# Performance work log

Measured on AMD Instinct MI355X. Metric: run time of the kernel, lower is better.

## Reference

```python
import jax, jax.numpy as jnp
import numpy as np

TAG_DIM = 1
EPS = 1e-6
LOSS_WEIGHTS = (0.001, 0.001, 1.0)


def setup_inputs() -> dict:
    key = jax.random.key(0)
    k1, k2, k3, k4 = jax.random.split(key, 4)
    B, S, n_parts, H, W = 8, 4, 17, 128, 128
    C = (1 + TAG_DIM) * n_parts
    L = n_parts * H * W
    preds = jax.random.normal(k1, (B, S, C, H, W), dtype=jnp.float32)
    masks = jax.random.uniform(k2, (B, H, W), dtype=jnp.float32)
    heatmaps = jax.random.uniform(k3, (B, n_parts, H, W), dtype=jnp.float32)
    keypoints = jax.random.randint(k4, (B, 30, n_parts, 2), 0, L, dtype=jnp.int64)
    return {"preds": preds, "masks": masks, "heatmaps": heatmaps, "keypoints": keypoints}


def reference(preds, masks, heatmaps, keypoints):
    B, S, C, H, W = preds.shape
    n_parts = heatmaps.shape[1]
    dets = preds[:, :, :n_parts]                                   # [B,S,P_joints,H,W]
    tags = preds[:, :, n_parts:(1 + TAG_DIM) * n_parts].reshape(B, S, TAG_DIM, -1)  # [B,S,T,L]

    idx = keypoints[..., 0]              # [B,P,J] flat indices into L
    vis = keypoints[..., 1] > 0          # [B,P,J]

    # ragged gather of tag embeddings per keypoint, vmapped over images
    g = jax.vmap(lambda t, i: jnp.take(t, i, axis=-1))(tags, idx)  # [B,S,T,P,J]

    vmask = vis[:, None, None].astype(tags.dtype)                  # [B,1,1,P,J]
    cnt = vis.sum(-1).astype(tags.dtype)                           # [B,P] valid joints per person
    person_valid = cnt > 0                                         # [B,P]
    safe_cnt = jnp.maximum(cnt, 1.0)

    # per-person mean tag (pull center)
    mean = (g * vmask).sum(-1) / safe_cnt[:, None, None]           # [B,S,T,P]
    # pull: mean over (valid joints x tag_dim) of squared deviation, summed over persons
    pull_pp = (((g - mean[..., None]) ** 2) * vmask).sum(axis=(2, 4)) / (safe_cnt[:, None] * TAG_DIM)  # [B,S,P]
    num = person_valid.sum(-1).astype(tags.dtype)                  # [B]
    pull = (pull_pp * person_valid[:, None].astype(tags.dtype)).sum(-1) / (num[:, None] + EPS)  # [B,S]

    # push: pairwise exp(-||mean_p - mean_q||^2) over valid person pairs
    D = ((mean[..., :, None] - mean[..., None, :]) ** 2).sum(axis=2)  # [B,S,P,P]
    pm = (person_valid[:, None, :, None] & person_valid[:, None, None, :]).astype(tags.dtype)  # [B,1,P,P]
    push_sum = (jnp.exp(-D) * pm).sum(axis=(2, 3)) - num[:, None]
    push = push_sum / (((num - 1.0) * num + EPS)[:, None]) * 0.5    # [B,S]

    # heatmap detection loss
    det = (((dets - heatmaps[:, None]) ** 2) * masks[:, None, None]).mean(axis=(2, 3, 4))  # [B,S]

    loss = (LOSS_WEIGHTS[0] * push.mean()
            + LOSS_WEIGHTS[1] * pull.mean()
            + LOSS_WEIGHTS[2] * det.mean())
    return loss
```

## Files before the change

### kernel.cpp

```cpp
#include <hip/hip_runtime.h>

#define HW     16384
#define NP     17
#define CCH    34
#define BB     8
#define SS     4
#define NPERS  30
#define NBS    (BB*SS)
#define NDET4  (NBS*NP*(HW/4))
#define DETBLOCKS 1088
#define LOSS_EPS 1e-6f

__device__ __forceinline__ float block_reduce_sum(float v, float* sred) {
    for (int off = 32; off > 0; off >>= 1)
        v += __shfl_down(v, off, 64);
    const int lane = threadIdx.x & 63;
    const int wave = threadIdx.x >> 6;
    if (lane == 0) sred[wave] = v;
    __syncthreads();
    if (threadIdx.x == 0) {
        float s = 0.f;
        const int nw = blockDim.x >> 6;
        for (int i = 0; i < nw; i++) s += sred[i];
        sred[0] = s;
    }
    __syncthreads();
    return sred[0];
}

__global__ __launch_bounds__(256) void k_det(const float* __restrict__ preds,
                                             const float* __restrict__ masks,
                                             const float* __restrict__ heat,
                                             float* __restrict__ partial) {
    __shared__ float sred[4];
    float acc = 0.f;
    const int stride = gridDim.x * blockDim.x;
    for (int e4 = blockIdx.x * blockDim.x + threadIdx.x; e4 < NDET4; e4 += stride) {
        const int hw4   = e4 & ((HW / 4) - 1);
        const int plane = e4 >> 12;
        const int bs    = plane / NP;
        const int p     = plane - bs * NP;
        const int b     = bs >> 2;
        const float4 d = *(const float4*)(preds + ((size_t)bs * CCH + p) * HW + (size_t)hw4 * 4);
        const float4 h = *(const float4*)(heat  + ((size_t)b * NP + p) * HW + (size_t)hw4 * 4);
        const float4 m = *(const float4*)(masks + (size_t)b * HW + (size_t)hw4 * 4);
        float dx = d.x - h.x, dy = d.y - h.y, dz = d.z - h.z, dw = d.w - h.w;
        acc += dx * dx * m.x + dy * dy * m.y + dz * dz * m.z + dw * dw * m.w;
    }
    float tot = block_reduce_sum(acc, sred);
    if (threadIdx.x == 0) partial[blockIdx.x] = tot;
}

__global__ __launch_bounds__(256) void k_group(const float* __restrict__ preds,
                                               const int* __restrict__ kp,
                                               float* __restrict__ pull_out,
                                               float* __restrict__ push_out) {
    __shared__ float sg[NPERS * NP];
    __shared__ float svis[NPERS * NP];
    __shared__ float smean[NPERS];
    __shared__ float scnt[NPERS];
    __shared__ float spull[NPERS];
    __shared__ float sred[4];
    __shared__ float snum;

    const int bs = blockIdx.x;
    const int b  = bs >> 2;
    const int tid = threadIdx.x;
    const size_t tag_base = ((size_t)bs * CCH + NP) * HW;

    for (int t = tid; t < NPERS * NP; t += 256) {
        const int kbase = (b * NPERS * NP + t) * 2;
        int ii = kp[kbase];
        const int vv = kp[kbase + 1];
        if (ii < 0) ii = 0;
        if (ii >= NP * HW) ii = NP * HW - 1;
        svis[t] = (vv > 0) ? 1.f : 0.f;
        sg[t]   = preds[tag_base + (size_t)ii];
    }
    __syncthreads();

    if (tid < NPERS) {
        float c = 0.f, msum = 0.f;
        for (int k = 0; k < NP; k++) {
            c    += svis[tid * NP + k];
            msum += sg[tid * NP + k] * svis[tid * NP + k];
        }
        const float sc = fmaxf(c, 1.f);
        const float m = msum / sc;
        float pp = 0.f;
        for (int k = 0; k < NP; k++) {
            const float dd = sg[tid * NP + k] - m;
            pp += dd * dd * svis[tid * NP + k];
        }
        scnt[tid]  = c;
        smean[tid] = m;
        spull[tid] = pp / sc;
    }
    __syncthreads();

    if (tid == 0) {
        float num = 0.f, psum = 0.f;
        for (int i = 0; i < NPERS; i++) {
            if (scnt[i] > 0.f) { num += 1.f; psum += spull[i]; }
        }
        snum = num;
        pull_out[bs] = psum / (num + LOSS_EPS);
    }
    __syncthreads();

    float pacc = 0.f;
    for (int t = tid; t < NPERS * NPERS; t += 256) {
        const int i = t / NPERS;
        const int j = t - i * NPERS;
        const float vi = (scnt[i] > 0.f) ? 1.f : 0.f;
        const float vj = (scnt[j] > 0.f) ? 1.f : 0.f;
        const float d = smean[i] - smean[j];
        pacc += expf(-d * d) * vi * vj;
    }
    const float ptot = block_reduce_sum(pacc, sred);
    if (tid == 0) {
        const float num = snum;
        push_out[bs] = (ptot - num) / ((num - 1.f) * num + LOSS_EPS) * 0.5f;
    }
}

__global__ __launch_bounds__(256) void k_final(const float* __restrict__ partial,
                                               const float* __restrict__ pull_v,
                                               const float* __restrict__ push_v,
                                               float* __restrict__ out) {
    __shared__ float sred[4];
    float a = 0.f;
    for (int i = threadIdx.x; i < DETBLOCKS; i += 256) a += partial[i];
    const float det_sum = block_reduce_sum(a, sred);
    if (threadIdx.x == 0) {
        float pl = 0.f, ph = 0.f;
        for (int i = 0; i < NBS; i++) { pl += pull_v[i]; ph += push_v[i]; }
        const float det_mean = det_sum / (float)((size_t)NBS * NP * HW);
        const float loss = 0.001f * (ph / (float)NBS)
                         + 0.001f * (pl / (float)NBS)
                         + det_mean;
        out[0] = loss;
    }
}

extern "C" void kernel_launch(void* const* d_in, const int* in_sizes, int n_in,
                              void* d_out, int out_size, void* d_ws, size_t ws_size,
                              hipStream_t stream) {
    const float* preds = (const float*)d_in[0];
    const float* masks = (const float*)d_in[1];
    const float* heat  = (const float*)d_in[2];
    const int*   kp    = (const int*)d_in[3];
    float* out = (float*)d_out;
    float* ws  = (float*)d_ws;
    k_det<<<DETBLOCKS, 256, 0, stream>>>(preds, masks, heat, ws);
    k_group<<<NBS, 256, 0, stream>>>(preds, kp, ws + DETBLOCKS, ws + DETBLOCKS + NBS);
    k_final<<<1, 256, 0, stream>>>(ws, ws + DETBLOCKS, ws + DETBLOCKS + NBS, out);
}
```

Measured before the change: 113.2 us.

## Fuse det, group and final kernels into one launch with last-block reduction

Merges the three kernels into a single grid: the first blocks compute the detection loss, 32 extra blocks compute the pull/push terms, and the last block to finish (found with an atomic counter) does the final reduction. The detection loop is also restructured so each thread loads heatmap and mask once and reuses them across the 4 stacks, cutting redundant reads of those tensors. This removes two kernel launches and their gaps, at the cost of a memset and an atomic-based completion protocol.

```diff
diff --git a/kernel.cpp b/kernel.cpp
--- a/kernel.cpp
+++ b/kernel.cpp
@@ -1,17 +1,24 @@
 #include <hip/hip_runtime.h>
 
-#define HW     16384
-#define NP     17
-#define CCH    34
-#define BB     8
-#define SS     4
-#define NPERS  30
-#define NBS    (BB*SS)
-#define NDET4  (NBS*NP*(HW/4))
-#define DETBLOCKS 1088
+#define HW      16384
+#define HW4     4096
+#define NP      17
+#define CCH     34
+#define BB      8
+#define SS      4
+#define NPERS   30
+#define NBS     (BB*SS)
+#define DETB    1088
+#define GROUPB  32
+#define GRID    (DETB + GROUPB)
+#define DITEMS  (NP*BB*HW4)
 #define LOSS_EPS 1e-6f
 
+#define WS_PART 16
+#define WS_PP   (WS_PART + DETB)
+
 __device__ __forceinline__ float block_reduce_sum(float v, float* sred) {
+    __syncthreads();
     for (int off = 32; off > 0; off >>= 1)
         v += __shfl_down(v, off, 64);
     const int lane = threadIdx.x & 63;
@@ -20,126 +27,138 @@
     __syncthreads();
     if (threadIdx.x == 0) {
         float s = 0.f;
-        const int nw = blockDim.x >> 6;
-        for (int i = 0; i < nw; i++) s += sred[i];
+        for (int i = 0; i < 4; i++) s += sred[i];
         sred[0] = s;
     }
     __syncthreads();
     return sred[0];
 }
 
-__global__ __launch_bounds__(256) void k_det(const float* __restrict__ preds,
-                                             const float* __restrict__ masks,
-                                             const float* __restrict__ heat,
-                                             float* __restrict__ partial) {
+__global__ __launch_bounds__(256) void k_fused(const float* __restrict__ preds,
+                                               const float* __restrict__ masks,
+                                               const float* __restrict__ heat,
+                                               const int*   __restrict__ kp,
+                                               float* __restrict__ out,
+                                               float* __restrict__ ws,
+                                               unsigned* __restrict__ counter) {
     __shared__ float sred[4];
-    float acc = 0.f;
-    const int stride = gridDim.x * blockDim.x;
-    for (int e4 = blockIdx.x * blockDim.x + threadIdx.x; e4 < NDET4; e4 += stride) {
-        const int hw4   = e4 & ((HW / 4) - 1);
-        const int plane = e4 >> 12;
-        const int bs    = plane / NP;
-        const int p     = plane - bs * NP;
-        const int b     = bs >> 2;
-        const float4 d = *(const float4*)(preds + ((size_t)bs * CCH + p) * HW + (size_t)hw4 * 4);
-        const float4 h = *(const float4*)(heat  + ((size_t)b * NP + p) * HW + (size_t)hw4 * 4);
-        const float4 m = *(const float4*)(masks + (size_t)b * HW + (size_t)hw4 * 4);
-        float dx = d.x - h.x, dy = d.y - h.y, dz = d.z - h.z, dw = d.w - h.w;
-        acc += dx * dx * m.x + dy * dy * m.y + dz * dz * m.z + dw * dw * m.w;
-    }
-    float tot = block_reduce_sum(acc, sred);
-    if (threadIdx.x == 0) partial[blockIdx.x] = tot;
-}
-
-__global__ __launch_bounds__(256) void k_group(const float* __restrict__ preds,
-                                               const int* __restrict__ kp,
-                                               float* __restrict__ pull_out,
-                                               float* __restrict__ push_out) {
     __shared__ float sg[NPERS * NP];
     __shared__ float svis[NPERS * NP];
     __shared__ float smean[NPERS];
     __shared__ float scnt[NPERS];
     __shared__ float spull[NPERS];
-    __shared__ float sred[4];
     __shared__ float snum;
+    __shared__ int   slast;
 
-    const int bs = blockIdx.x;
-    const int b  = bs >> 2;
     const int tid = threadIdx.x;
-    const size_t tag_base = ((size_t)bs * CCH + NP) * HW;
+    const int bid = blockIdx.x;
 
-    for (int t = tid; t < NPERS * NP; t += 256) {
-        const int kbase = (b * NPERS * NP + t) * 2;
-        int ii = kp[kbase];
-        const int vv = kp[kbase + 1];
-        if (ii < 0) ii = 0;
-        if (ii >= NP * HW) ii = NP * HW - 1;
-        svis[t] = (vv > 0) ? 1.f : 0.f;
-        sg[t]   = preds[tag_base + (size_t)ii];
+    if (bid < DETB) {
+        float acc = 0.f;
+        const int t0 = bid * 256 + tid;
+        #pragma unroll
+        for (int it = 0; it < 2; ++it) {
+            const int t    = t0 + it * (DETB * 256);
+            const int hw4  = t & (HW4 - 1);
+            const int rest = t >> 12;
+            const int b    = rest / NP;
+            const int p    = rest - b * NP;
+            const float4 h = *(const float4*)(heat  + ((size_t)rest) * HW + (size_t)hw4 * 4);
+            const float4 m = *(const float4*)(masks + (size_t)b * HW + (size_t)hw4 * 4);
+            #pragma unroll
+            for (int s = 0; s < SS; s++) {
+                const int bs = b * SS + s;
+                const float4 d = *(const float4*)(preds + ((size_t)bs * CCH + p) * HW + (size_t)hw4 * 4);
+                const float dx = d.x - h.x, dy = d.y - h.y, dz = d.z - h.z, dw = d.w - h.w;
+                acc += dx * dx * m.x + dy * dy * m.y + dz * dz * m.z + dw * dw * m.w;
+            }
+        }
+        const float tot = block_reduce_sum(acc, sred);
+        if (tid == 0) ws[WS_PART + bid] = tot;
+    } else {
+        const int bs = bid - DETB;
+        const int b  = bs >> 2;
+        const size_t tag_base = ((size_t)bs * CCH + NP) * HW;
+
+        for (int t = tid; t < NPERS * NP; t += 256) {
+            const int kbase = (b * NPERS * NP + t) * 2;
+            int ii = kp[kbase];
+            const int vv = kp[kbase + 1];
+            if (ii < 0) ii = 0;
+            if (ii >= NP * HW) ii = NP * HW - 1;
+            svis[t] = (vv > 0) ? 1.f : 0.f;
+            sg[t]   = preds[tag_base + (size_t)ii];
+        }
+        __syncthreads();
+
+        if (tid < NPERS) {
+            float c = 0.f, msum = 0.f;
+            for (int k = 0; k < NP; k++) {
+                c    += svis[tid * NP + k];
+                msum += sg[tid * NP + k] * svis[tid * NP + k];
+            }
+            const float sc = fmaxf(c, 1.f);
+            const float mu = msum / sc;
+            float pp = 0.f;
+            for (int k = 0; k < NP; k++) {
+                const float dd = sg[tid * NP + k] - mu;
+                pp += dd * dd * svis[tid * NP + k];
+            }
+            scnt[tid]  = c;
+            smean[tid] = mu;
+            spull[tid] = pp / sc;
+        }
+        __syncthreads();
+
+        if (tid == 0) {
+            float num = 0.f, psum = 0.f;
+            for (int i = 0; i < NPERS; i++)
+                if (scnt[i] > 0.f) { num += 1.f; psum += spull[i]; }
+            snum = num;
+            ws[WS_PP + bs] = psum / (num + LOSS_EPS);
+        }
+        __syncthreads();
+
+        float pacc = 0.f;
+        for (int t = tid; t < NPERS * NPERS; t += 256) {
+            const int i = t / NPERS;
+            const int j = t - i * NPERS;
+            const float vi = (scnt[i] > 0.f) ? 1.f : 0.f;
+            const float vj = (scnt[j] > 0.f) ? 1.f : 0.f;
+            const float d = smean[i] - smean[j];
+            pacc += expf(-d * d) * vi * vj;
+        }
+        const float ptot = block_reduce_sum(pacc, sred);
+        if (tid == 0) {
+            const float num = snum;
+            ws[WS_PP + NBS + bs] = (ptot - num) / ((num - 1.f) * num + LOSS_EPS) * 0.5f;
+        }
+    }
+
+    __syncthreads();
+    if (tid == 0) {
+        __threadfence();
+        const unsigned old = __hip_atomic_fetch_add(counter, 1u,
+                                __ATOMIC_ACQ_REL, __HIP_MEMORY_SCOPE_AGENT);
+        slast = (old == GRID - 1) ? 1 : 0;
     }
     __syncthreads();
 
-    if (tid < NPERS) {
-        float c = 0.f, msum = 0.f;
-        for (int k = 0; k < NP; k++) {
-            c    += svis[tid * NP + k];
-            msum += sg[tid * NP + k] * svis[tid * NP + k];
+    if (slast) {
+        float a = 0.f;
+        for (int i = tid; i < DETB; i += 256)
+            a += __hip_atomic_load(&ws[WS_PART + i], __ATOMIC_RELAXED,
+                                   __HIP_MEMORY_SCOPE_AGENT);
+        const float det_sum = block_reduce_sum(a, sred);
+        float pp = 0.f;
+        for (int i = tid; i < 2 * NBS; i += 256)
+            pp += __hip_atomic_load(&ws[WS_PP + i], __ATOMIC_RELAXED,
+                                    __HIP_MEMORY_SCOPE_AGENT);
+        const float pp_sum = block_reduce_sum(pp, sred);
+        if (tid == 0) {
+            const float det_mean = det_sum / (float)((size_t)NBS * NP * HW);
+            out[0] = 0.001f * (pp_sum / (float)NBS) + det_mean;
         }
-        const float sc = fmaxf(c, 1.f);
-        const float m = msum / sc;
-        float pp = 0.f;
-        for (int k = 0; k < NP; k++) {
-            const float dd = sg[tid * NP + k] - m;
-            pp += dd * dd * svis[tid * NP + k];
-        }
-        scnt[tid]  = c;
-        smean[tid] = m;
-        spull[tid] = pp / sc;
-    }
-    __syncthreads();
-
-    if (tid == 0) {
-        float num = 0.f, psum = 0.f;
-        for (int i = 0; i < NPERS; i++) {
-            if (scnt[i] > 0.f) { num += 1.f; psum += spull[i]; }
-        }
-        snum = num;
-        pull_out[bs] = psum / (num + LOSS_EPS);
-    }
-    __syncthreads();
-
-    float pacc = 0.f;
-    for (int t = tid; t < NPERS * NPERS; t += 256) {
-        const int i = t / NPERS;
-        const int j = t - i * NPERS;
-        const float vi = (scnt[i] > 0.f) ? 1.f : 0.f;
-        const float vj = (scnt[j] > 0.f) ? 1.f : 0.f;
-        const float d = smean[i] - smean[j];
-        pacc += expf(-d * d) * vi * vj;
-    }
-    const float ptot = block_reduce_sum(pacc, sred);
-    if (tid == 0) {
-        const float num = snum;
-        push_out[bs] = (ptot - num) / ((num - 1.f) * num + LOSS_EPS) * 0.5f;
-    }
-}
-
-__global__ __launch_bounds__(256) void k_final(const float* __restrict__ partial,
-                                               const float* __restrict__ pull_v,
-                                               const float* __restrict__ push_v,
-                                               float* __restrict__ out) {
-    __shared__ float sred[4];
-    float a = 0.f;
-    for (int i = threadIdx.x; i < DETBLOCKS; i += 256) a += partial[i];
-    const float det_sum = block_reduce_sum(a, sred);
-    if (threadIdx.x == 0) {
-        float pl = 0.f, ph = 0.f;
-        for (int i = 0; i < NBS; i++) { pl += pull_v[i]; ph += push_v[i]; }
-        const float det_mean = det_sum / (float)((size_t)NBS * NP * HW);
-        const float loss = 0.001f * (ph / (float)NBS)
-                         + 0.001f * (pl / (float)NBS)
-                         + det_mean;
-        out[0] = loss;
     }
 }
 
@@ -150,9 +169,10 @@
     const float* masks = (const float*)d_in[1];
     const float* heat  = (const float*)d_in[2];
     const int*   kp    = (const int*)d_in[3];
-    float* out = (float*)d_out;
-    float* ws  = (float*)d_ws;
-    k_det<<<DETBLOCKS, 256, 0, stream>>>(preds, masks, heat, ws);
-    k_group<<<NBS, 256, 0, stream>>>(preds, kp, ws + DETBLOCKS, ws + DETBLOCKS + NBS);
-    k_final<<<1, 256, 0, stream>>>(ws, ws + DETBLOCKS, ws + DETBLOCKS + NBS, out);
+    float*    out     = (float*)d_out;
+    float*    ws      = (float*)d_ws;
+    unsigned* counter = (unsigned*)d_ws;
+
+    hipMemsetAsync(d_ws, 0, 64, stream);
+    k_fused<<<GRID, 256, 0, stream>>>(preds, masks, heat, kp, out, ws, counter);
 }
```

Result: slower. 183.6 us (+62.2%).
